# Performance work log

Measured on AMD Instinct MI355X. Metric: run time of the kernel, lower is better.

## Reference

```python
import jax, jax.numpy as jnp
import numpy as np

EMBED_DIM = 1024
NUM_HEADS = 16
HEAD_DIM = EMBED_DIM // NUM_HEADS


def setup_inputs() -> dict:
    key = jax.random.key(0)
    ks = jax.random.split(key, 8)
    B, S, D = 2, 2048, EMBED_DIM
    scale = 1.0 / np.sqrt(D)
    return {
        "query": jax.random.normal(ks[0], (B, S, D), dtype=jnp.float32),
        "key": jax.random.normal(ks[1], (B, S, D), dtype=jnp.float32),
        "value": jax.random.normal(ks[2], (B, S, D), dtype=jnp.float32),
        "Wq": jax.random.normal(ks[3], (D, D), dtype=jnp.float32) * scale,
        "Wk": jax.random.normal(ks[4], (D, D), dtype=jnp.float32) * scale,
        "Wv": jax.random.normal(ks[5], (D, D), dtype=jnp.float32) * scale,
        "Wo": jax.random.normal(ks[6], (D, D), dtype=jnp.float32) * scale,
        "attention_mask": jax.random.randint(ks[7], (B, S), 0, 2, dtype=jnp.int32),
    }


def reference(query, key, value, Wq, Wk, Wv, Wo, attention_mask):
    B, Sq, D = query.shape
    Sk = key.shape[1]
    H, hd = NUM_HEADS, HEAD_DIM
    # linear projections (no bias), split into heads: [B, H, S, hd]
    q = (query @ Wq).reshape(B, Sq, H, hd).transpose(0, 2, 1, 3)
    k = (key @ Wk).reshape(B, Sk, H, hd).transpose(0, 2, 1, 3)
    v = (value @ Wv).reshape(B, Sk, H, hd).transpose(0, 2, 1, 3)
    # scaled dot-product scores: [B, H, Sq, Sk]; scale uses head_dim (post-split key dim)
    scores = jnp.einsum("bhqd,bhkd->bhqk", q, k) / jnp.sqrt(jnp.float32(hd))
    # padding mask [B, Sk] broadcast to [B, 1, 1, Sk]; 0 -> -inf
    mask = attention_mask[:, None, None, :]
    scores = jnp.where(mask == 0, -jnp.inf, scores)
    weights = jax.nn.softmax(scores, axis=-1)
    out = jnp.einsum("bhqk,bhkd->bhqd", weights, v)  # [B, H, Sq, hd]
    out = out.transpose(0, 2, 1, 3).reshape(B, Sq, D)
    return out @ Wo
```

## Files before the change

### kernel.cpp

```cpp
#include <hip/hip_runtime.h>
#include <hip/hip_bf16.h>

typedef short bf16x8 __attribute__((ext_vector_type(8)));
typedef float f32x4 __attribute__((ext_vector_type(4)));

#define S_LEN 2048
#define NHEAD 16
#define DM 1024

#if __has_builtin(__builtin_amdgcn_exp2f)
#define EXP2(x) __builtin_amdgcn_exp2f(x)
#else
#define EXP2(x) exp2f(x)
#endif

__device__ __forceinline__ short f2bf(float f) {
  union { float f; unsigned u; } x; x.f = f;
  unsigned r = x.u + 0x7fffu + ((x.u >> 16) & 1u);
  return (short)(r >> 16);
}

__device__ __forceinline__ unsigned cvt_pk_bf16(float lo, float hi) {
  unsigned r;
  asm("v_cvt_pk_bf16_f32 %0, %1, %2" : "=v"(r) : "v"(lo), "v"(hi));
  return r;
}

__device__ __forceinline__ void pl32swap(unsigned& a, unsigned& b) {
#if __has_builtin(__builtin_amdgcn_permlane32_swap)
  auto r = __builtin_amdgcn_permlane32_swap(a, b, false, false);
  a = r[0]; b = r[1];
#else
  asm volatile("v_permlane32_swap_b32 %0, %1" : "+v"(a), "+v"(b));
#endif
}
__device__ __forceinline__ void pl16swap(unsigned& a, unsigned& b) {
#if __has_builtin(__builtin_amdgcn_permlane16_swap)
  auto r = __builtin_amdgcn_permlane16_swap(a, b, false, false);
  a = r[0]; b = r[1];
#else
  asm volatile("v_permlane16_swap_b32 %0, %1" : "+v"(a), "+v"(b));
#endif
}

__device__ __forceinline__ void gload16(const void* g, void* l) {
  __builtin_amdgcn_global_load_lds(
      (const __attribute__((address_space(1))) void*)g,
      (__attribute__((address_space(3))) void*)l, 16, 0, 0);
}

__global__ __launch_bounds__(256) void wtrans(const float* __restrict__ Wq, const float* __restrict__ Wk,
                                              const float* __restrict__ Wv, const float* __restrict__ Wo,
                                              short* Tq, short* Tk, short* Tv, short* To) {
  const int z = blockIdx.z;
  const float* W = (z == 0) ? Wq : (z == 1) ? Wk : (z == 2) ? Wv : Wo;
  short* T = (z == 0) ? Tq : (z == 1) ? Tk : (z == 2) ? Tv : To;
  __shared__ short Tl[64][72];
  const int tid = threadIdx.x;
  const int k0 = blockIdx.x * 64, n0 = blockIdx.y * 64;
  const int r = tid >> 2, c0 = (tid & 3) * 16;
#pragma unroll
  for (int j = 0; j < 4; j++) {
    float4 v = *(const float4*)&W[(size_t)(k0 + r) * DM + n0 + c0 + 4 * j];
    Tl[r][c0 + 4 * j + 0] = f2bf(v.x);
    Tl[r][c0 + 4 * j + 1] = f2bf(v.y);
    Tl[r][c0 + 4 * j + 2] = f2bf(v.z);
    Tl[r][c0 + 4 * j + 3] = f2bf(v.w);
  }
  __syncthreads();
  bf16x8 o0, o1;
#pragma unroll
  for (int j = 0; j < 8; j++) { o0[j] = Tl[c0 + j][r]; o1[j] = Tl[c0 + 8 + j][r]; }
  *(bf16x8*)&T[(size_t)(n0 + r) * DM + k0 + c0] = o0;
  *(bf16x8*)&T[(size_t)(n0 + r) * DM + k0 + c0 + 8] = o1;
}

__global__ __launch_bounds__(256) void xcvt(const float* __restrict__ q, const float* __restrict__ k,
                                            const float* __restrict__ v,
                                            short* xq, short* xk, short* xv) {
  const int z = blockIdx.y;
  const float* src = (z == 0) ? q : (z == 1) ? k : v;
  short* dst = (z == 0) ? xq : (z == 1) ? xk : xv;
  const size_t base = ((size_t)blockIdx.x * 256 + threadIdx.x) * 16;
  float4 a = *(const float4*)&src[base];
  float4 b = *(const float4*)&src[base + 4];
  float4 c = *(const float4*)&src[base + 8];
  float4 d = *(const float4*)&src[base + 12];
  bf16x8 o0, o1;
  o0[0] = f2bf(a.x); o0[1] = f2bf(a.y); o0[2] = f2bf(a.z); o0[3] = f2bf(a.w);
  o0[4] = f2bf(b.x); o0[5] = f2bf(b.y); o0[6] = f2bf(b.z); o0[7] = f2bf(b.w);
  o1[0] = f2bf(c.x); o1[1] = f2bf(c.y); o1[2] = f2bf(c.z); o1[3] = f2bf(c.w);
  o1[4] = f2bf(d.x); o1[5] = f2bf(d.y); o1[6] = f2bf(d.z); o1[7] = f2bf(d.w);
  *(bf16x8*)&dst[base] = o0;
  *(bf16x8*)&dst[base + 8] = o1;
}

template<int CM>
__global__ __launch_bounds__(256) void gemm3(const short* __restrict__ A, const short* __restrict__ Bt,
                                             void* __restrict__ Cp, int M, int N, int K) {
  __shared__ __align__(16) short Al[2][128 * 64];
  __shared__ __align__(16) short Bl[2][64 * 64];
  const int tid = threadIdx.x;
  const int lane = tid & 63, w = tid >> 6;
  const int wm = w >> 1, wn = w & 1;
  const int lr = lane & 15, g = lane >> 4;

  const int flat = blockIdx.y * gridDim.x + blockIdx.x;
  const int nwg = gridDim.x * gridDim.y;
  const int wid = (flat & 7) * (nwg >> 3) + (flat >> 3);
  const int bx = wid % gridDim.x, by = wid / gridDim.x;
  const int m0 = by * 128, n0 = bx * 64;

  f32x4 acc[4][2];
#pragma unroll
  for (int i = 0; i < 4; i++)
#pragma unroll
    for (int j = 0; j < 2; j++) acc[i][j] = (f32x4){0.f, 0.f, 0.f, 0.f};

  const int srow = lane >> 3;
  const int sch = (lane & 7) ^ (srow & 7);
  const short* gA = A + (size_t)(m0 + w * 32 + srow) * K + 8 * sch;
  const short* gB = Bt + (size_t)(n0 + w * 16 + srow) * K + 8 * sch;

#define STAGE(buf, kk)                                                              \
  do {                                                                              \
    _Pragma("unroll") for (int c = 0; c < 4; c++)                                   \
        gload16(gA + (size_t)c * 8 * K + (kk), &Al[buf][(w * 32 + c * 8) * 64]);    \
    _Pragma("unroll") for (int c = 0; c < 2; c++)                                   \
        gload16(gB + (size_t)c * 8 * K + (kk), &Bl[buf][(w * 16 + c * 8) * 64]);    \
  } while (0)

  const int nsteps = K >> 6;
  STAGE(0, 0);
  int buf = 0;
  for (int t = 0; t < nsteps; t++) {
    __syncthreads();
    if (t + 1 < nsteps) STAGE(buf ^ 1, (t + 1) << 6);
#pragma unroll
    for (int kc = 0; kc < 2; kc++) {
      bf16x8 af[4], bfr[2];
#pragma unroll
      for (int mt = 0; mt < 4; mt++) {
        int row = wm * 64 + mt * 16 + lr;
        af[mt] = *(const bf16x8*)&Al[buf][row * 64 + 8 * ((kc * 4 + g) ^ (lr & 7))];
      }
#pragma unroll
      for (int nt = 0; nt < 2; nt++) {
        int row = wn * 32 + nt * 16 + lr;
        bfr[nt] = *(const bf16x8*)&Bl[buf][row * 64 + 8 * ((kc * 4 + g) ^ (lr & 7))];
      }
      __builtin_amdgcn_s_setprio(1);
#pragma unroll
      for (int mt = 0; mt < 4; mt++)
#pragma unroll
        for (int nt = 0; nt < 2; nt++)
          acc[mt][nt] = __builtin_amdgcn_mfma_f32_16x16x32_bf16(af[mt], bfr[nt], acc[mt][nt], 0, 0, 0);
      __builtin_amdgcn_s_setprio(0);
    }
    buf ^= 1;
  }
#undef STAGE

#pragma unroll
  for (int mt = 0; mt < 4; mt++)
#pragma unroll
    for (int nt = 0; nt < 2; nt++)
#pragma unroll
      for (int r = 0; r < 4; r++) {
        int row = m0 + wm * 64 + mt * 16 + g * 4 + r;
        int col = n0 + wn * 32 + nt * 16 + lr;
        if (CM == 0) {
          ((float*)Cp)[(size_t)row * N + col] = acc[mt][nt][r];
        } else if (CM == 1 || CM == 3) {
          float v = (CM == 3) ? acc[mt][nt][r] * 0.18033688011f : acc[mt][nt][r];
          int b = row >> 11, s = row & (S_LEN - 1);
          int h = col >> 6, d = col & 63;
          ((short*)Cp)[(((size_t)(b * NHEAD + h)) * S_LEN + s) * 64 + d] = f2bf(v);
        } else {
          int h = row >> 6, d = row & 63;
          int b = col >> 11, s = col & (S_LEN - 1);
          ((short*)Cp)[(((size_t)(b * NHEAD + h)) * 64 + d) * S_LEN + s] = f2bf(acc[mt][nt][r]);
        }
      }
}

template<int AM, int BMODE, int CM>
__global__ __launch_bounds__(256) void gemm2(const void* __restrict__ Ap, const void* __restrict__ Bp,
                                             void* __restrict__ Cp, int M, int N, int K) {
  __shared__ __align__(16) short Al[128][72];
  __shared__ __align__(16) short Bl[64][72];
  const int tid = threadIdx.x;
  const int lane = tid & 63, w = tid >> 6;
  const int wm = w >> 1, wn = w & 1;
  const int lr = lane & 15, g = lane >> 4;
  const int m0 = blockIdx.y * 128, n0 = blockIdx.x * 64;

  f32x4 acc[4][2];
#pragma unroll
  for (int i = 0; i < 4; i++)
#pragma unroll
    for (int j = 0; j < 2; j++) acc[i][j] = (f32x4){0.f, 0.f, 0.f, 0.f};

  const int ar = tid >> 1, ac = (tid & 1) * 32;
  const int br = tid >> 2, bc = (tid & 3) * 16;

  float4 la[8]; bf16x8 la8[4];
  float4 lb[4]; bf16x8 lb8[2];

#define LOADA(kk)                                                                        \
  do {                                                                                   \
    if (AM == 0) {                                                                       \
      const float* A = (const float*)Ap;                                                 \
      _Pragma("unroll") for (int j = 0; j < 8; j++)                                      \
          la[j] = *(const float4*)&A[(size_t)(m0 + ar) * K + (kk) + ac + 4 * j];         \
    } else {                                                                             \
      const short* A = (const short*)Ap;                                                 \
      _Pragma("unroll") for (int j = 0; j < 4; j++)                                      \
          la8[j] = *(const bf16x8*)&A[(size_t)(m0 + ar) * K + (kk) + ac + 8 * j];        \
    }                                                                                    \
  } while (0)

#define LOADB(kk)                                                                        \
  do {                                                                                   \
    if (BMODE == 0) {                                                                    \
      const float* B = (const float*)Bp;                                                 \
      _Pragma("unroll") for (int j = 0; j < 4; j++)                                      \
          lb[j] = *(const float4*)&B[(size_t)(n0 + br) * K + (kk) + bc + 4 * j];         \
    } else if (BMODE == 1) {                                                             \
      const short* B = (const short*)Bp;                                                 \
      _Pragma("unroll") for (int j = 0; j < 2; j++)                                      \
          lb8[j] = *(const bf16x8*)&B[(size_t)(n0 + br) * K + (kk) + bc + 8 * j];        \
    } else {                                                                             \
      const float* B = (const float*)Bp;                                                 \
      _Pragma("unroll") for (int j = 0; j < 4; j++)                                      \
          lb[j] = *(const float4*)&B[(size_t)((kk) + br) * N + n0 + bc + 4 * j];         \
    }                                                                                    \
  } while (0)

  const int nsteps = K >> 6;
  LOADA(0); LOADB(0);

  for (int t = 0; t < nsteps; t++) {
    __syncthreads();
    if (AM == 0) {
#pragma unroll
      for (int j = 0; j < 4; j++) {
        float4 v0 = la[2 * j], v1 = la[2 * j + 1];
        bf16x8 tt;
        tt[0] = f2bf(v0.x); tt[1] = f2bf(v0.y); tt[2] = f2bf(v0.z); tt[3] = f2bf(v0.w);
        tt[4] = f2bf(v1.x); tt[5] = f2bf(v1.y); tt[6] = f2bf(v1.z); tt[7] = f2bf(v1.w);
        *(bf16x8*)&Al[ar][ac + 8 * j] = tt;
      }
    } else {
#pragma unroll
      for (int j = 0; j < 4; j++) *(bf16x8*)&Al[ar][ac + 8 * j] = la8[j];
    }
    if (BMODE == 0) {
#pragma unroll
      for (int j = 0; j < 2; j++) {
        float4 v0 = lb[2 * j], v1 = lb[2 * j + 1];
        bf16x8 tt;
        tt[0] = f2bf(v0.x); tt[1] = f2bf(v0.y); tt[2] = f2bf(v0.z); tt[3] = f2bf(v0.w);
        tt[4] = f2bf(v1.x); tt[5] = f2bf(v1.y); tt[6] = f2bf(v1.z); tt[7] = f2bf(v1.w);
        *(bf16x8*)&Bl[br][bc + 8 * j] = tt;
      }
    } else if (BMODE == 1) {
#pragma unroll
      for (int j = 0; j < 2; j++) *(bf16x8*)&Bl[br][bc + 8 * j] = lb8[j];
    } else {
#pragma unroll
      for (int j = 0; j < 4; j++) {
        float4 v = lb[j];
        Bl[bc + 4 * j + 0][br] = f2bf(v.x);
        Bl[bc + 4 * j + 1][br] = f2bf(v.y);
        Bl[bc + 4 * j + 2][br] = f2bf(v.z);
        Bl[bc + 4 * j + 3][br] = f2bf(v.w);
      }
    }
    __syncthreads();
    if (t + 1 < nsteps) { LOADA((t + 1) << 6); LOADB((t + 1) << 6); }
#pragma unroll
    for (int kc = 0; kc < 2; kc++) {
      bf16x8 af[4], bfr[2];
#pragma unroll
      for (int mt = 0; mt < 4; mt++) af[mt] = *(const bf16x8*)&Al[wm * 64 + mt * 16 + lr][kc * 32 + g * 8];
#pragma unroll
      for (int nt = 0; nt < 2; nt++) bfr[nt] = *(const bf16x8*)&Bl[wn * 32 + nt * 16 + lr][kc * 32 + g * 8];
#pragma unroll
      for (int mt = 0; mt < 4; mt++)
#pragma unroll
        for (int nt = 0; nt < 2; nt++)
          acc[mt][nt] = __builtin_amdgcn_mfma_f32_16x16x32_bf16(af[mt], bfr[nt], acc[mt][nt], 0, 0, 0);
    }
  }
#undef LOADA
#undef LOADB

#pragma unroll
  for (int mt = 0; mt < 4; mt++)
#pragma unroll
    for (int nt = 0; nt < 2; nt++)
#pragma unroll
      for (int r = 0; r < 4; r++) {
        int row = m0 + wm * 64 + mt * 16 + g * 4 + r;
        int col = n0 + wn * 32 + nt * 16 + lr;
        if (CM == 0) {
          ((float*)Cp)[(size_t)row * N + col] = acc[mt][nt][r];
        } else if (CM == 1 || CM == 3) {
          float v = (CM == 3) ? acc[mt][nt][r] * 0.18033688011f : acc[mt][nt][r];
          int b = row >> 11, s = row & (S_LEN - 1);
          int h = col >> 6, d = col & 63;
          ((short*)Cp)[(((size_t)(b * NHEAD + h)) * S_LEN + s) * 64 + d] = f2bf(v);
        } else {
          int h = row >> 6, d = row & 63;
          int b = col >> 11, s = col & (S_LEN - 1);
          ((short*)Cp)[(((size_t)(b * NHEAD + h)) * 64 + d) * S_LEN + s] = f2bf(acc[mt][nt][r]);
        }
      }
}

__global__ __launch_bounds__(256, 2) void attn6(const short* __restrict__ Qb,
                                                const short* __restrict__ Kb,
                                                const short* __restrict__ VbT,
                                                const int* __restrict__ mask,
                                                short* __restrict__ Ob) {
  __shared__ __align__(16) short Kl[2][64][64];
  __shared__ __align__(16) short Vl[2][64][64];

  const int tid = threadIdx.x;
  const int lane = tid & 63, w = tid >> 6;
  const int lr = lane & 15, g = lane >> 4;

  const int flat = blockIdx.y * gridDim.x + blockIdx.x;
  const int wid = (flat & 7) * 64 + (flat >> 3);
  const int qblk = wid & 15, bh = wid >> 4;
  const int b = bh >> 4, h = bh & 15;
  const int qbase = qblk * 128;
  const size_t hoff = (size_t)bh * S_LEN * 64;

  bf16x8 qf[2][2];
#pragma unroll
  for (int qfr = 0; qfr < 2; qfr++)
#pragma unroll
    for (int kh = 0; kh < 2; kh++)
      qf[qfr][kh] = *(const bf16x8*)&Qb[hoff + (size_t)(qbase + w * 32 + qfr * 16 + lr) * 64 + kh * 32 + g * 8];

  f32x4 o_acc[2][4];
  float lsum[2];
#pragma unroll
  for (int qfr = 0; qfr < 2; qfr++) {
    lsum[qfr] = 0.f;
#pragma unroll
    for (int dg = 0; dg < 4; dg++) o_acc[qfr][dg] = (f32x4){0.f, 0.f, 0.f, 0.f};
  }

  const int* maskb = mask + b * S_LEN;
  const int srow = lane >> 3;
  const int sch = (lane & 7) ^ (srow & 7);
  const short* gK = Kb + hoff + (size_t)(w * 16 + srow) * 64 + 8 * sch;
  const short* gV = VbT + hoff + (size_t)(w * 16 + srow) * S_LEN + 8 * sch;

#define STAGEKV(buf, kb)                                                         \
  do {                                                                           \
    _Pragma("unroll") for (int c = 0; c < 2; c++)                                \
        gload16(gK + (size_t)(kb + c * 8) * 64, &Kl[buf][w * 16 + c * 8][0]);    \
    _Pragma("unroll") for (int c = 0; c < 2; c++)                                \
        gload16(gV + (size_t)c * 8 * S_LEN + (kb), &Vl[buf][w * 16 + c * 8][0]); \
  } while (0)

  const int NT = S_LEN / 64;
  STAGEKV(0, 0);
  int buf = 0;

  for (int t = 0; t < NT; t++) {
    const int kb = t * 64;
    __syncthreads();
    if (t + 1 < NT) STAGEKV(buf ^ 1, kb + 64);

    float bias[4][4];
#pragma unroll
    for (int nt = 0; nt < 4; nt++) {
      int4 mv = *(const int4*)&maskb[kb + nt * 16 + 4 * g];
      bias[nt][0] = mv.x ? 0.f : -1e30f;
      bias[nt][1] = mv.y ? 0.f : -1e30f;
      bias[nt][2] = mv.z ? 0.f : -1e30f;
      bias[nt][3] = mv.w ? 0.f : -1e30f;
    }

    bf16x8 kfr[4][2];
#pragma unroll
    for (int nt = 0; nt < 4; nt++)
#pragma unroll
      for (int kh = 0; kh < 2; kh++)
        kfr[nt][kh] = *(const bf16x8*)&Kl[buf][nt * 16 + lr][8 * ((4 * kh + g) ^ (lr & 7))];

    bf16x8 vfr[4][2];
#pragma unroll
    for (int dg = 0; dg < 4; dg++)
#pragma unroll
      for (int kh = 0; kh < 2; kh++)
        vfr[dg][kh] = *(const bf16x8*)&Vl[buf][dg * 16 + lr][8 * ((4 * kh + g) ^ (lr & 7))];

#pragma unroll
    for (int qfr = 0; qfr < 2; qfr++) {
      f32x4 s[4];
#pragma unroll
      for (int nt = 0; nt < 4; nt++) s[nt] = (f32x4){0.f, 0.f, 0.f, 0.f};
      __builtin_amdgcn_s_setprio(1);
#pragma unroll
      for (int nt = 0; nt < 4; nt++) {
        s[nt] = __builtin_amdgcn_mfma_f32_16x16x32_bf16(kfr[nt][0], qf[qfr][0], s[nt], 0, 0, 0);
        s[nt] = __builtin_amdgcn_mfma_f32_16x16x32_bf16(kfr[nt][1], qf[qfr][1], s[nt], 0, 0, 0);
      }
      __builtin_amdgcn_s_setprio(0);

      unsigned W0[4], W1[4];
#pragma unroll
      for (int nt = 0; nt < 4; nt++) {
        float p0 = EXP2(s[nt][0] + bias[nt][0]);
        float p1 = EXP2(s[nt][1] + bias[nt][1]);
        float p2 = EXP2(s[nt][2] + bias[nt][2]);
        float p3 = EXP2(s[nt][3] + bias[nt][3]);
        lsum[qfr] += (p0 + p1) + (p2 + p3);
        W0[nt] = cvt_pk_bf16(p0, p1);
        W1[nt] = cvt_pk_bf16(p2, p3);
      }

      bf16x8 pf[2];
#pragma unroll
      for (int kh = 0; kh < 2; kh++) {
        unsigned a0 = W0[2 * kh], b0 = W0[2 * kh + 1];
        unsigned a1 = W1[2 * kh], b1 = W1[2 * kh + 1];
        pl32swap(a0, b0); pl16swap(a0, b0);
        pl32swap(a1, b1); pl16swap(a1, b1);
        union { unsigned u[4]; bf16x8 v; } pk;
        pk.u[0] = a0; pk.u[1] = a1; pk.u[2] = b0; pk.u[3] = b1;
        pf[kh] = pk.v;
      }

      __builtin_amdgcn_s_setprio(1);
#pragma unroll
      for (int dg = 0; dg < 4; dg++) {
        o_acc[qfr][dg] = __builtin_amdgcn_mfma_f32_16x16x32_bf16(pf[0], vfr[dg][0], o_acc[qfr][dg], 0, 0, 0);
        o_acc[qfr][dg] = __builtin_amdgcn_mfma_f32_16x16x32_bf16(pf[1], vfr[dg][1], o_acc[qfr][dg], 0, 0, 0);
      }
      __builtin_amdgcn_s_setprio(0);
    }
    buf ^= 1;
  }
#undef STAGEKV

#pragma unroll
  for (int qfr = 0; qfr < 2; qfr++) {
    float l = lsum[qfr];
    l += __shfl_xor(l, 16);
    l += __shfl_xor(l, 32);
    float inv = 1.f / l;
    float invq[4];
#pragma unroll
    for (int r = 0; r < 4; r++) invq[r] = __shfl(inv, 4 * g + r);
#pragma unroll
    for (int dg = 0; dg < 4; dg++)
#pragma unroll
      for (int r = 0; r < 4; r++) {
        int qr = qbase + w * 32 + qfr * 16 + 4 * g + r;
        int col = h * 64 + dg * 16 + lr;
        Ob[((size_t)b * S_LEN + qr) * DM + col] = f2bf(o_acc[qfr][dg][r] * invq[r]);
      }
  }
}

extern "C" void kernel_launch(void* const* d_in, const int* in_sizes, int n_in,
                              void* d_out, int out_size, void* d_ws, size_t ws_size,
                              hipStream_t stream) {
  const float* query = (const float*)d_in[0];
  const float* key   = (const float*)d_in[1];
  const float* value = (const float*)d_in[2];
  const float* Wq = (const float*)d_in[3];
  const float* Wk = (const float*)d_in[4];
  const float* Wv = (const float*)d_in[5];
  const float* Wo = (const float*)d_in[6];
  const int* mask = (const int*)d_in[7];

  char* ws = (char*)d_ws;
  const size_t MB = 1 << 20;
  const bool big = ws_size >= 41 * MB;

  dim3 ag(S_LEN / 128, 2 * NHEAD);

  if (big) {
    short* xq  = (short*)(ws);
    short* xk  = (short*)(ws + 8 * MB);
    short* xv  = (short*)(ws + 16 * MB);
    short* WqT = (short*)(ws + 24 * MB);
    short* WkT = (short*)(ws + 26 * MB);
    short* WvT = (short*)(ws + 28 * MB);
    short* WoT = (short*)(ws + 30 * MB);
    short* Qb  = (short*)(ws + 32 * MB);
    short* Kb  = xq;
    short* VbT = xk;
    short* Ob  = xv;

    dim3 tgrid(16, 16, 4);
    wtrans<<<tgrid, 256, 0, stream>>>(Wq, Wk, Wv, Wo, WqT, WkT, WvT, WoT);
    dim3 cg(1024, 3);
    xcvt<<<cg, 256, 0, stream>>>(query, key, value, xq, xk, xv);

    dim3 gqk(DM / 64, (2 * S_LEN) / 128);
    gemm3<3><<<gqk, 256, 0, stream>>>(xq, WqT, Qb, 2 * S_LEN, DM, DM);
    gemm3<1><<<gqk, 256, 0, stream>>>(xk, WkT, Kb, 2 * S_LEN, DM, DM);
    dim3 gv((2 * S_LEN) / 64, DM / 128);
    gemm3<2><<<gv, 256, 0, stream>>>(WvT, xv, VbT, DM, 2 * S_LEN, DM);

    attn6<<<ag, 256, 0, stream>>>(Qb, Kb, VbT, mask, Ob);

    gemm3<0><<<gqk, 256, 0, stream>>>(Ob, WoT, (float*)d_out, 2 * S_LEN, DM, DM);
  } else {
    short* Qb  = (short*)(ws);
    short* Kb  = (short*)(ws + 8 * MB);
    short* VbT = (short*)(ws + 16 * MB);
    short* WqT = (short*)(ws + 24 * MB);
    short* WkT = (short*)(ws + 26 * MB);
    short* WvT = (short*)(ws + 28 * MB);
    short* Ob  = (short*)(ws + 24 * MB);

    dim3 tgrid(16, 16, 3);
    wtrans<<<tgrid, 256, 0, stream>>>(Wq, Wk, Wv, Wo, WqT, WkT, WvT, WqT);

    dim3 gq(DM / 64, (2 * S_LEN) / 128);
    gemm2<0, 1, 3><<<gq, 256, 0, stream>>>(query, WqT, Qb, 2 * S_LEN, DM, DM);
    gemm2<0, 1, 1><<<gq, 256, 0, stream>>>(key,   WkT, Kb, 2 * S_LEN, DM, DM);
    dim3 gv((2 * S_LEN) / 64, DM / 128);
    gemm2<1, 0, 2><<<gv, 256, 0, stream>>>(WvT, value, VbT, DM, 2 * S_LEN, DM);

    attn6<<<ag, 256, 0, stream>>>(Qb, Kb, VbT, mask, Ob);

    gemm2<1, 2, 0><<<gq, 256, 0, stream>>>(Ob, Wo, (float*)d_out, 2 * S_LEN, DM, DM);
  }
}
```

Before: 137.4 us.

## Fuse fp32 conversion into a single QKV projection GEMM and retile attention

Replaces the separate fp32-to-bf16 conversion kernel and three projection GEMMs with one kernel, gemm4. It reads fp32 activations directly, converts them into LDS, and uses the concatenated transposed Wq/Wk/Wv weights to write Q (pre-scaled), K and transposed V. This removes the intermediate bf16 activation round trip through memory and several kernel launches. Attention is retiled from 128 to 64 queries per block, with one query fragment per wave and higher declared occupancy. That gives the grid more blocks to spread across CUs, at the cost of less reuse of each staged K/V tile.

```diff
diff --git a/kernel.cpp b/kernel.cpp
--- a/kernel.cpp
+++ b/kernel.cpp
@@ -75,24 +75,113 @@
   *(bf16x8*)&T[(size_t)(n0 + r) * DM + k0 + c0 + 8] = o1;
 }
 
-__global__ __launch_bounds__(256) void xcvt(const float* __restrict__ q, const float* __restrict__ k,
-                                            const float* __restrict__ v,
-                                            short* xq, short* xk, short* xv) {
-  const int z = blockIdx.y;
-  const float* src = (z == 0) ? q : (z == 1) ? k : v;
-  short* dst = (z == 0) ? xq : (z == 1) ? xk : xv;
-  const size_t base = ((size_t)blockIdx.x * 256 + threadIdx.x) * 16;
-  float4 a = *(const float4*)&src[base];
-  float4 b = *(const float4*)&src[base + 4];
-  float4 c = *(const float4*)&src[base + 8];
-  float4 d = *(const float4*)&src[base + 12];
-  bf16x8 o0, o1;
-  o0[0] = f2bf(a.x); o0[1] = f2bf(a.y); o0[2] = f2bf(a.z); o0[3] = f2bf(a.w);
-  o0[4] = f2bf(b.x); o0[5] = f2bf(b.y); o0[6] = f2bf(b.z); o0[7] = f2bf(b.w);
-  o1[0] = f2bf(c.x); o1[1] = f2bf(c.y); o1[2] = f2bf(c.z); o1[3] = f2bf(c.w);
-  o1[4] = f2bf(d.x); o1[5] = f2bf(d.y); o1[6] = f2bf(d.z); o1[7] = f2bf(d.w);
-  *(bf16x8*)&dst[base] = o0;
-  *(bf16x8*)&dst[base + 8] = o1;
+__global__ __launch_bounds__(256) void gemm4(const float* __restrict__ xq, const float* __restrict__ xk,
+                                             const float* __restrict__ xv, const short* __restrict__ Wt,
+                                             short* __restrict__ Qb, short* __restrict__ Kb,
+                                             short* __restrict__ VbT) {
+  __shared__ __align__(16) short Al[128 * 64];
+  __shared__ __align__(16) short Bl[2][64 * 64];
+  const int tid = threadIdx.x;
+  const int lane = tid & 63, w = tid >> 6;
+  const int wm = w >> 1, wn = w & 1;
+  const int lr = lane & 15, g = lane >> 4;
+
+  const int flat = blockIdx.y * gridDim.x + blockIdx.x;
+  const int wid = (flat & 7) * 192 + (flat >> 3);
+  const int bx = wid % 48, by = wid / 48;
+  const int n0 = bx * 64, m0 = by * 128;
+  const int which = n0 >> 10;
+  const float* A = (which == 0) ? xq : (which == 1) ? xk : xv;
+
+  f32x4 acc[4][2];
+#pragma unroll
+  for (int i = 0; i < 4; i++)
+#pragma unroll
+    for (int j = 0; j < 2; j++) acc[i][j] = (f32x4){0.f, 0.f, 0.f, 0.f};
+
+  const int ar = tid >> 1, ac = (tid & 1) * 32;
+  float4 la[8];
+  const int srow = lane >> 3;
+  const int sch = (lane & 7) ^ (srow & 7);
+  const short* gB = Wt + (size_t)(n0 + w * 16 + srow) * 1024 + 8 * sch;
+
+#define LOADA4(kk)                                                                  \
+  do {                                                                              \
+    _Pragma("unroll") for (int j = 0; j < 8; j++)                                   \
+        la[j] = *(const float4*)&A[(size_t)(m0 + ar) * 1024 + (kk) + ac + 4 * j];   \
+  } while (0)
+#define STAGEB(buf, kk)                                                             \
+  do {                                                                              \
+    _Pragma("unroll") for (int c = 0; c < 2; c++)                                   \
+        gload16(gB + (size_t)c * 8 * 1024 + (kk), &Bl[buf][(w * 16 + c * 8) * 64]); \
+  } while (0)
+
+  const int nsteps = 16;
+  LOADA4(0);
+  STAGEB(0, 0);
+  int buf = 0;
+  for (int t = 0; t < nsteps; t++) {
+    __syncthreads();
+#pragma unroll
+    for (int j = 0; j < 4; j++) {
+      float4 v0 = la[2 * j], v1 = la[2 * j + 1];
+      bf16x8 tt;
+      tt[0] = f2bf(v0.x); tt[1] = f2bf(v0.y); tt[2] = f2bf(v0.z); tt[3] = f2bf(v0.w);
+      tt[4] = f2bf(v1.x); tt[5] = f2bf(v1.y); tt[6] = f2bf(v1.z); tt[7] = f2bf(v1.w);
+      *(bf16x8*)&Al[ar * 64 + 8 * (((ac >> 3) + j) ^ (ar & 7))] = tt;
+    }
+    __syncthreads();
+    if (t + 1 < nsteps) { STAGEB(buf ^ 1, (t + 1) << 6); LOADA4((t + 1) << 6); }
+#pragma unroll
+    for (int kc = 0; kc < 2; kc++) {
+      bf16x8 af[4], bfr[2];
+#pragma unroll
+      for (int mt = 0; mt < 4; mt++) {
+        int row = wm * 64 + mt * 16 + lr;
+        af[mt] = *(const bf16x8*)&Al[row * 64 + 8 * ((kc * 4 + g) ^ (lr & 7))];
+      }
+#pragma unroll
+      for (int nt = 0; nt < 2; nt++) {
+        int row = wn * 32 + nt * 16 + lr;
+        bfr[nt] = *(const bf16x8*)&Bl[buf][row * 64 + 8 * ((kc * 4 + g) ^ (lr & 7))];
+      }
+      __builtin_amdgcn_s_setprio(1);
+#pragma unroll
+      for (int mt = 0; mt < 4; mt++)
+#pragma unroll
+        for (int nt = 0; nt < 2; nt++)
+          acc[mt][nt] = __builtin_amdgcn_mfma_f32_16x16x32_bf16(af[mt], bfr[nt], acc[mt][nt], 0, 0, 0);
+      __builtin_amdgcn_s_setprio(0);
+    }
+    buf ^= 1;
+  }
+#undef LOADA4
+#undef STAGEB
+
+  const int hcol = (n0 >> 6) & 15;
+#pragma unroll
+  for (int mt = 0; mt < 4; mt++)
+#pragma unroll
+    for (int nt = 0; nt < 2; nt++) {
+      const int d = wn * 32 + nt * 16 + lr;
+      if (which == 2) {
+        const int sb = m0 + wm * 64 + mt * 16 + g * 4;
+        const int bb = sb >> 11, s = sb & (S_LEN - 1);
+        union { short s4[4]; uint2 u; } pk;
+#pragma unroll
+        for (int r = 0; r < 4; r++) pk.s4[r] = f2bf(acc[mt][nt][r]);
+        *(uint2*)&VbT[(((size_t)(bb * NHEAD + hcol)) * 64 + d) * S_LEN + s] = pk.u;
+      } else {
+        short* dst = (which == 0) ? Qb : Kb;
+        const float scale = (which == 0) ? 0.18033688011f : 1.f;
+#pragma unroll
+        for (int r = 0; r < 4; r++) {
+          int row = m0 + wm * 64 + mt * 16 + g * 4 + r;
+          int bb = row >> 11, s = row & (S_LEN - 1);
+          dst[(((size_t)(bb * NHEAD + hcol)) * S_LEN + s) * 64 + d] = f2bf(acc[mt][nt][r] * scale);
+        }
+      }
+    }
 }
 
 template<int CM>
@@ -319,7 +408,7 @@
       }
 }
 
-__global__ __launch_bounds__(256, 2) void attn6(const short* __restrict__ Qb,
+__global__ __launch_bounds__(256, 4) void attn7(const short* __restrict__ Qb,
                                                 const short* __restrict__ Kb,
                                                 const short* __restrict__ VbT,
                                                 const int* __restrict__ mask,
@@ -332,27 +421,21 @@
   const int lr = lane & 15, g = lane >> 4;
 
   const int flat = blockIdx.y * gridDim.x + blockIdx.x;
-  const int wid = (flat & 7) * 64 + (flat >> 3);
-  const int qblk = wid & 15, bh = wid >> 4;
+  const int wid = (flat & 7) * 128 + (flat >> 3);
+  const int qblk = wid & 31, bh = wid >> 5;
   const int b = bh >> 4, h = bh & 15;
-  const int qbase = qblk * 128;
+  const int qbase = qblk * 64;
   const size_t hoff = (size_t)bh * S_LEN * 64;
 
-  bf16x8 qf[2][2];
-#pragma unroll
-  for (int qfr = 0; qfr < 2; qfr++)
-#pragma unroll
-    for (int kh = 0; kh < 2; kh++)
-      qf[qfr][kh] = *(const bf16x8*)&Qb[hoff + (size_t)(qbase + w * 32 + qfr * 16 + lr) * 64 + kh * 32 + g * 8];
-
-  f32x4 o_acc[2][4];
-  float lsum[2];
-#pragma unroll
-  for (int qfr = 0; qfr < 2; qfr++) {
-    lsum[qfr] = 0.f;
-#pragma unroll
-    for (int dg = 0; dg < 4; dg++) o_acc[qfr][dg] = (f32x4){0.f, 0.f, 0.f, 0.f};
-  }
+  bf16x8 qf[2];
+#pragma unroll
+  for (int kh = 0; kh < 2; kh++)
+    qf[kh] = *(const bf16x8*)&Qb[hoff + (size_t)(qbase + w * 16 + lr) * 64 + kh * 32 + g * 8];
+
+  f32x4 o_acc[4];
+  float lsum = 0.f;
+#pragma unroll
+  for (int dg = 0; dg < 4; dg++) o_acc[dg] = (f32x4){0.f, 0.f, 0.f, 0.f};
 
   const int* maskb = mask + b * S_LEN;
   const int srow = lane >> 3;
@@ -387,72 +470,58 @@
       bias[nt][3] = mv.w ? 0.f : -1e30f;
     }
 
-    bf16x8 kfr[4][2];
-#pragma unroll
-    for (int nt = 0; nt < 4; nt++)
-#pragma unroll
-      for (int kh = 0; kh < 2; kh++)
-        kfr[nt][kh] = *(const bf16x8*)&Kl[buf][nt * 16 + lr][8 * ((4 * kh + g) ^ (lr & 7))];
-
-    bf16x8 vfr[4][2];
-#pragma unroll
-    for (int dg = 0; dg < 4; dg++)
-#pragma unroll
-      for (int kh = 0; kh < 2; kh++)
-        vfr[dg][kh] = *(const bf16x8*)&Vl[buf][dg * 16 + lr][8 * ((4 * kh + g) ^ (lr & 7))];
-
-#pragma unroll
-    for (int qfr = 0; qfr < 2; qfr++) {
-      f32x4 s[4];
-#pragma unroll
-      for (int nt = 0; nt < 4; nt++) s[nt] = (f32x4){0.f, 0.f, 0.f, 0.f};
-      __builtin_amdgcn_s_setprio(1);
-#pragma unroll
-      for (int nt = 0; nt < 4; nt++) {
-        s[nt] = __builtin_amdgcn_mfma_f32_16x16x32_bf16(kfr[nt][0], qf[qfr][0], s[nt], 0, 0, 0);
-        s[nt] = __builtin_amdgcn_mfma_f32_16x16x32_bf16(kfr[nt][1], qf[qfr][1], s[nt], 0, 0, 0);
-      }
-      __builtin_amdgcn_s_setprio(0);
-
-      unsigned W0[4], W1[4];
-#pragma unroll
-      for (int nt = 0; nt < 4; nt++) {
-        float p0 = EXP2(s[nt][0] + bias[nt][0]);
-        float p1 = EXP2(s[nt][1] + bias[nt][1]);
-        float p2 = EXP2(s[nt][2] + bias[nt][2]);
-        float p3 = EXP2(s[nt][3] + bias[nt][3]);
-        lsum[qfr] += (p0 + p1) + (p2 + p3);
-        W0[nt] = cvt_pk_bf16(p0, p1);
-        W1[nt] = cvt_pk_bf16(p2, p3);
-      }
-
-      bf16x8 pf[2];
-#pragma unroll
-      for (int kh = 0; kh < 2; kh++) {
-        unsigned a0 = W0[2 * kh], b0 = W0[2 * kh + 1];
-        unsigned a1 = W1[2 * kh], b1 = W1[2 * kh + 1];
-        pl32swap(a0, b0); pl16swap(a0, b0);
-        pl32swap(a1, b1); pl16swap(a1, b1);
-        union { unsigned u[4]; bf16x8 v; } pk;
-        pk.u[0] = a0; pk.u[1] = a1; pk.u[2] = b0; pk.u[3] = b1;
-        pf[kh] = pk.v;
-      }
-
-      __builtin_amdgcn_s_setprio(1);
-#pragma unroll
-      for (int dg = 0; dg < 4; dg++) {
-        o_acc[qfr][dg] = __builtin_amdgcn_mfma_f32_16x16x32_bf16(pf[0], vfr[dg][0], o_acc[qfr][dg], 0, 0, 0);
-        o_acc[qfr][dg] = __builtin_amdgcn_mfma_f32_16x16x32_bf16(pf[1], vfr[dg][1], o_acc[qfr][dg], 0, 0, 0);
-      }
-      __builtin_amdgcn_s_setprio(0);
-    }
+    f32x4 s[4];
+#pragma unroll
+    for (int nt = 0; nt < 4; nt++) s[nt] = (f32x4){0.f, 0.f, 0.f, 0.f};
+    __builtin_amdgcn_s_setprio(1);
+#pragma unroll
+    for (int nt = 0; nt < 4; nt++) {
+      bf16x8 k0 = *(const bf16x8*)&Kl[buf][nt * 16 + lr][8 * (g ^ (lr & 7))];
+      bf16x8 k1 = *(const bf16x8*)&Kl[buf][nt * 16 + lr][8 * ((4 + g) ^ (lr & 7))];
+      s[nt] = __builtin_amdgcn_mfma_f32_16x16x32_bf16(k0, qf[0], s[nt], 0, 0, 0);
+      s[nt] = __builtin_amdgcn_mfma_f32_16x16x32_bf16(k1, qf[1], s[nt], 0, 0, 0);
+    }
+    __builtin_amdgcn_s_setprio(0);
+
+    unsigned W0[4], W1[4];
+#pragma unroll
+    for (int nt = 0; nt < 4; nt++) {
+      float p0 = EXP2(s[nt][0] + bias[nt][0]);
+      float p1 = EXP2(s[nt][1] + bias[nt][1]);
+      float p2 = EXP2(s[nt][2] + bias[nt][2]);
+      float p3 = EXP2(s[nt][3] + bias[nt][3]);
+      lsum += (p0 + p1) + (p2 + p3);
+      W0[nt] = cvt_pk_bf16(p0, p1);
+      W1[nt] = cvt_pk_bf16(p2, p3);
+    }
+
+    bf16x8 pf[2];
+#pragma unroll
+    for (int kh = 0; kh < 2; kh++) {
+      unsigned a0 = W0[2 * kh], b0 = W0[2 * kh + 1];
+      unsigned a1 = W1[2 * kh], b1 = W1[2 * kh + 1];
+      pl32swap(a0, b0); pl16swap(a0, b0);
+      pl32swap(a1, b1); pl16swap(a1, b1);
+      union { unsigned u[4]; bf16x8 v; } pk;
+      pk.u[0] = a0; pk.u[1] = a1; pk.u[2] = b0; pk.u[3] = b1;
+      pf[kh] = pk.v;
+    }
+
+    __builtin_amdgcn_s_setprio(1);
+#pragma unroll
+    for (int dg = 0; dg < 4; dg++) {
+      bf16x8 v0 = *(const bf16x8*)&Vl[buf][dg * 16 + lr][8 * (g ^ (lr & 7))];
+      bf16x8 v1 = *(const bf16x8*)&Vl[buf][dg * 16 + lr][8 * ((4 + g) ^ (lr & 7))];
+      o_acc[dg] = __builtin_amdgcn_mfma_f32_16x16x32_bf16(pf[0], v0, o_acc[dg], 0, 0, 0);
+      o_acc[dg] = __builtin_amdgcn_mfma_f32_16x16x32_bf16(pf[1], v1, o_acc[dg], 0, 0, 0);
+    }
+    __builtin_amdgcn_s_setprio(0);
     buf ^= 1;
   }
 #undef STAGEKV
 
-#pragma unroll
-  for (int qfr = 0; qfr < 2; qfr++) {
-    float l = lsum[qfr];
+  {
+    float l = lsum;
     l += __shfl_xor(l, 16);
     l += __shfl_xor(l, 32);
     float inv = 1.f / l;
@@ -463,9 +532,9 @@
     for (int dg = 0; dg < 4; dg++)
 #pragma unroll
       for (int r = 0; r < 4; r++) {
-        int qr = qbase + w * 32 + qfr * 16 + 4 * g + r;
+        int qr = qbase + w * 16 + 4 * g + r;
         int col = h * 64 + dg * 16 + lr;
-        Ob[((size_t)b * S_LEN + qr) * DM + col] = f2bf(o_acc[qfr][dg][r] * invq[r]);
+        Ob[((size_t)b * S_LEN + qr) * DM + col] = f2bf(o_acc[dg][r] * invq[r]);
       }
   }
 }
@@ -486,34 +555,27 @@
   const size_t MB = 1 << 20;
   const bool big = ws_size >= 41 * MB;
 
-  dim3 ag(S_LEN / 128, 2 * NHEAD);
+  dim3 ag(S_LEN / 64, 2 * NHEAD);
 
   if (big) {
-    short* xq  = (short*)(ws);
-    short* xk  = (short*)(ws + 8 * MB);
-    short* xv  = (short*)(ws + 16 * MB);
+    short* Qb  = (short*)(ws);
+    short* Kb  = (short*)(ws + 8 * MB);
+    short* VbT = (short*)(ws + 16 * MB);
     short* WqT = (short*)(ws + 24 * MB);
     short* WkT = (short*)(ws + 26 * MB);
     short* WvT = (short*)(ws + 28 * MB);
     short* WoT = (short*)(ws + 30 * MB);
-    short* Qb  = (short*)(ws + 32 * MB);
-    short* Kb  = xq;
-    short* VbT = xk;
-    short* Ob  = xv;
+    short* Ob  = (short*)(ws + 32 * MB);
 
     dim3 tgrid(16, 16, 4);
     wtrans<<<tgrid, 256, 0, stream>>>(Wq, Wk, Wv, Wo, WqT, WkT, WvT, WoT);
-    dim3 cg(1024, 3);
-    xcvt<<<cg, 256, 0, stream>>>(query, key, value, xq, xk, xv);
+
+    dim3 gqkv(48, 32);
+    gemm4<<<gqkv, 256, 0, stream>>>(query, key, value, WqT, Qb, Kb, VbT);
+
+    attn7<<<ag, 256, 0, stream>>>(Qb, Kb, VbT, mask, Ob);
 
     dim3 gqk(DM / 64, (2 * S_LEN) / 128);
-    gemm3<3><<<gqk, 256, 0, stream>>>(xq, WqT, Qb, 2 * S_LEN, DM, DM);
-    gemm3<1><<<gqk, 256, 0, stream>>>(xk, WkT, Kb, 2 * S_LEN, DM, DM);
-    dim3 gv((2 * S_LEN) / 64, DM / 128);
-    gemm3<2><<<gv, 256, 0, stream>>>(WvT, xv, VbT, DM, 2 * S_LEN, DM);
-
-    attn6<<<ag, 256, 0, stream>>>(Qb, Kb, VbT, mask, Ob);
-
     gemm3<0><<<gqk, 256, 0, stream>>>(Ob, WoT, (float*)d_out, 2 * S_LEN, DM, DM);
   } else {
     short* Qb  = (short*)(ws);
@@ -533,7 +595,7 @@
     dim3 gv((2 * S_LEN) / 64, DM / 128);
     gemm2<1, 0, 2><<<gv, 256, 0, stream>>>(WvT, value, VbT, DM, 2 * S_LEN, DM);
 
-    attn6<<<ag, 256, 0, stream>>>(Qb, Kb, VbT, mask, Ob);
+    attn7<<<ag, 256, 0, stream>>>(Qb, Kb, VbT, mask, Ob);
 
     gemm2<1, 2, 0><<<gq, 256, 0, stream>>>(Ob, Wo, (float*)d_out, 2 * S_LEN, DM, DM);
   }
```

Measured after the change: 188.1 us. +36.9%, slower.

## Shrink attention query tile and fold padding mask into V and MFMA denominator

Applied to the files above, without the earlier changes.

The attention kernel now handles 64 query rows per block, one 16-row fragment per wave, and allows 4 blocks per CU, so the grid doubles and per-thread register use drops. The padding mask is applied once in the V projection epilogue by zeroing masked value columns. It is also precomputed as a bf16 0/1 vector, and the softmax denominator comes from an extra MFMA against that vector instead of per-element bias adds and scalar row sums. This removes mask loads and adds from the inner loop, but each block now reuses each K/V tile for half as many query rows, which raises total K/V staging traffic. The small-workspace path gets a matching single-fragment kernel that keeps the bias-based masking.

```diff
diff --git a/kernel.cpp b/kernel.cpp
--- a/kernel.cpp
+++ b/kernel.cpp
@@ -51,12 +51,20 @@
 
 __global__ __launch_bounds__(256) void wtrans(const float* __restrict__ Wq, const float* __restrict__ Wk,
                                               const float* __restrict__ Wv, const float* __restrict__ Wo,
-                                              short* Tq, short* Tk, short* Tv, short* To) {
+                                              const int* __restrict__ mask,
+                                              short* Tq, short* Tk, short* Tv, short* To, short* Mb) {
   const int z = blockIdx.z;
+  const int tid = threadIdx.x;
+  if (z == 4) {
+    if (blockIdx.y == 0 && blockIdx.x < 16) {
+      int i = blockIdx.x * 256 + tid;
+      Mb[i] = mask[i] ? (short)0x3F80 : (short)0;
+    }
+    return;
+  }
   const float* W = (z == 0) ? Wq : (z == 1) ? Wk : (z == 2) ? Wv : Wo;
   short* T = (z == 0) ? Tq : (z == 1) ? Tk : (z == 2) ? Tv : To;
   __shared__ short Tl[64][72];
-  const int tid = threadIdx.x;
   const int k0 = blockIdx.x * 64, n0 = blockIdx.y * 64;
   const int r = tid >> 2, c0 = (tid & 3) * 16;
 #pragma unroll
@@ -97,7 +105,8 @@
 
 template<int CM>
 __global__ __launch_bounds__(256) void gemm3(const short* __restrict__ A, const short* __restrict__ Bt,
-                                             void* __restrict__ Cp, int M, int N, int K) {
+                                             void* __restrict__ Cp, int M, int N, int K,
+                                             const int* __restrict__ mask) {
   __shared__ __align__(16) short Al[2][128 * 64];
   __shared__ __align__(16) short Bl[2][64 * 64];
   const int tid = threadIdx.x;
@@ -164,24 +173,37 @@
 #pragma unroll
   for (int mt = 0; mt < 4; mt++)
 #pragma unroll
-    for (int nt = 0; nt < 2; nt++)
-#pragma unroll
-      for (int r = 0; r < 4; r++) {
-        int row = m0 + wm * 64 + mt * 16 + g * 4 + r;
-        int col = n0 + wn * 32 + nt * 16 + lr;
-        if (CM == 0) {
+    for (int nt = 0; nt < 2; nt++) {
+      if (CM == 0) {
+#pragma unroll
+        for (int r = 0; r < 4; r++) {
+          int row = m0 + wm * 64 + mt * 16 + g * 4 + r;
+          int col = n0 + wn * 32 + nt * 16 + lr;
           ((float*)Cp)[(size_t)row * N + col] = acc[mt][nt][r];
-        } else if (CM == 1 || CM == 3) {
-          float v = (CM == 3) ? acc[mt][nt][r] * 0.18033688011f : acc[mt][nt][r];
+        }
+      } else if (CM == 1 || CM == 3) {
+        const float scale = (CM == 3) ? 0.18033688011f : 1.f;
+#pragma unroll
+        for (int r = 0; r < 4; r++) {
+          int row = m0 + wm * 64 + mt * 16 + g * 4 + r;
+          int col = n0 + wn * 32 + nt * 16 + lr;
           int b = row >> 11, s = row & (S_LEN - 1);
           int h = col >> 6, d = col & 63;
-          ((short*)Cp)[(((size_t)(b * NHEAD + h)) * S_LEN + s) * 64 + d] = f2bf(v);
-        } else {
+          ((short*)Cp)[(((size_t)(b * NHEAD + h)) * S_LEN + s) * 64 + d] = f2bf(acc[mt][nt][r] * scale);
+        }
+      } else {
+#pragma unroll
+        for (int r = 0; r < 4; r++) {
+          int row = m0 + wm * 64 + mt * 16 + g * 4 + r;
+          int col = n0 + wn * 32 + nt * 16 + lr;
           int h = row >> 6, d = row & 63;
           int b = col >> 11, s = col & (S_LEN - 1);
-          ((short*)Cp)[(((size_t)(b * NHEAD + h)) * 64 + d) * S_LEN + s] = f2bf(acc[mt][nt][r]);
+          float v = acc[mt][nt][r];
+          if (CM == 4) v = mask[b * S_LEN + s] ? v : 0.f;
+          ((short*)Cp)[(((size_t)(b * NHEAD + h)) * 64 + d) * S_LEN + s] = f2bf(v);
         }
       }
+    }
 }
 
 template<int AM, int BMODE, int CM>
@@ -319,10 +341,10 @@
       }
 }
 
-__global__ __launch_bounds__(256, 2) void attn6(const short* __restrict__ Qb,
+__global__ __launch_bounds__(256, 4) void attn8(const short* __restrict__ Qb,
                                                 const short* __restrict__ Kb,
                                                 const short* __restrict__ VbT,
-                                                const int* __restrict__ mask,
+                                                const short* __restrict__ Mb,
                                                 short* __restrict__ Ob) {
   __shared__ __align__(16) short Kl[2][64][64];
   __shared__ __align__(16) short Vl[2][64][64];
@@ -332,29 +354,23 @@
   const int lr = lane & 15, g = lane >> 4;
 
   const int flat = blockIdx.y * gridDim.x + blockIdx.x;
-  const int wid = (flat & 7) * 64 + (flat >> 3);
-  const int qblk = wid & 15, bh = wid >> 4;
+  const int wid = (flat & 7) * 128 + (flat >> 3);
+  const int qblk = wid & 31, bh = wid >> 5;
   const int b = bh >> 4, h = bh & 15;
-  const int qbase = qblk * 128;
+  const int qbase = qblk * 64;
   const size_t hoff = (size_t)bh * S_LEN * 64;
 
-  bf16x8 qf[2][2];
-#pragma unroll
-  for (int qfr = 0; qfr < 2; qfr++)
-#pragma unroll
-    for (int kh = 0; kh < 2; kh++)
-      qf[qfr][kh] = *(const bf16x8*)&Qb[hoff + (size_t)(qbase + w * 32 + qfr * 16 + lr) * 64 + kh * 32 + g * 8];
-
-  f32x4 o_acc[2][4];
-  float lsum[2];
-#pragma unroll
-  for (int qfr = 0; qfr < 2; qfr++) {
-    lsum[qfr] = 0.f;
-#pragma unroll
-    for (int dg = 0; dg < 4; dg++) o_acc[qfr][dg] = (f32x4){0.f, 0.f, 0.f, 0.f};
-  }
-
-  const int* maskb = mask + b * S_LEN;
+  bf16x8 qf[2];
+#pragma unroll
+  for (int kh = 0; kh < 2; kh++)
+    qf[kh] = *(const bf16x8*)&Qb[hoff + (size_t)(qbase + w * 16 + lr) * 64 + kh * 32 + g * 8];
+
+  f32x4 o_acc[4];
+  f32x4 o_l = (f32x4){0.f, 0.f, 0.f, 0.f};
+#pragma unroll
+  for (int dg = 0; dg < 4; dg++) o_acc[dg] = (f32x4){0.f, 0.f, 0.f, 0.f};
+
+  const short* Mbb = Mb + b * S_LEN;
   const int srow = lane >> 3;
   const int sch = (lane & 7) ^ (srow & 7);
   const short* gK = Kb + hoff + (size_t)(w * 16 + srow) * 64 + 8 * sch;
@@ -374,6 +390,123 @@
 
   for (int t = 0; t < NT; t++) {
     const int kb = t * 64;
+    bf16x8 mf0 = *(const bf16x8*)&Mbb[kb + g * 8];
+    bf16x8 mf1 = *(const bf16x8*)&Mbb[kb + 32 + g * 8];
+    __syncthreads();
+    if (t + 1 < NT) STAGEKV(buf ^ 1, kb + 64);
+
+    f32x4 s[4];
+#pragma unroll
+    for (int nt = 0; nt < 4; nt++) s[nt] = (f32x4){0.f, 0.f, 0.f, 0.f};
+    __builtin_amdgcn_s_setprio(1);
+#pragma unroll
+    for (int nt = 0; nt < 4; nt++) {
+      bf16x8 k0 = *(const bf16x8*)&Kl[buf][nt * 16 + lr][8 * (g ^ (lr & 7))];
+      bf16x8 k1 = *(const bf16x8*)&Kl[buf][nt * 16 + lr][8 * ((4 + g) ^ (lr & 7))];
+      s[nt] = __builtin_amdgcn_mfma_f32_16x16x32_bf16(k0, qf[0], s[nt], 0, 0, 0);
+      s[nt] = __builtin_amdgcn_mfma_f32_16x16x32_bf16(k1, qf[1], s[nt], 0, 0, 0);
+    }
+    __builtin_amdgcn_s_setprio(0);
+
+    unsigned W0[4], W1[4];
+#pragma unroll
+    for (int nt = 0; nt < 4; nt++) {
+      float p0 = EXP2(s[nt][0]);
+      float p1 = EXP2(s[nt][1]);
+      float p2 = EXP2(s[nt][2]);
+      float p3 = EXP2(s[nt][3]);
+      W0[nt] = cvt_pk_bf16(p0, p1);
+      W1[nt] = cvt_pk_bf16(p2, p3);
+    }
+
+    bf16x8 pf[2];
+#pragma unroll
+    for (int kh = 0; kh < 2; kh++) {
+      unsigned a0 = W0[2 * kh], b0 = W0[2 * kh + 1];
+      unsigned a1 = W1[2 * kh], b1 = W1[2 * kh + 1];
+      pl32swap(a0, b0); pl16swap(a0, b0);
+      pl32swap(a1, b1); pl16swap(a1, b1);
+      union { unsigned u[4]; bf16x8 v; } pk;
+      pk.u[0] = a0; pk.u[1] = a1; pk.u[2] = b0; pk.u[3] = b1;
+      pf[kh] = pk.v;
+    }
+
+    __builtin_amdgcn_s_setprio(1);
+#pragma unroll
+    for (int dg = 0; dg < 4; dg++) {
+      bf16x8 v0 = *(const bf16x8*)&Vl[buf][dg * 16 + lr][8 * (g ^ (lr & 7))];
+      bf16x8 v1 = *(const bf16x8*)&Vl[buf][dg * 16 + lr][8 * ((4 + g) ^ (lr & 7))];
+      o_acc[dg] = __builtin_amdgcn_mfma_f32_16x16x32_bf16(pf[0], v0, o_acc[dg], 0, 0, 0);
+      o_acc[dg] = __builtin_amdgcn_mfma_f32_16x16x32_bf16(pf[1], v1, o_acc[dg], 0, 0, 0);
+    }
+    o_l = __builtin_amdgcn_mfma_f32_16x16x32_bf16(pf[0], mf0, o_l, 0, 0, 0);
+    o_l = __builtin_amdgcn_mfma_f32_16x16x32_bf16(pf[1], mf1, o_l, 0, 0, 0);
+    __builtin_amdgcn_s_setprio(0);
+    buf ^= 1;
+  }
+#undef STAGEKV
+
+#pragma unroll
+  for (int r = 0; r < 4; r++) {
+    float inv = 1.f / o_l[r];
+    int qr = qbase + w * 16 + 4 * g + r;
+#pragma unroll
+    for (int dg = 0; dg < 4; dg++) {
+      int col = h * 64 + dg * 16 + lr;
+      Ob[((size_t)b * S_LEN + qr) * DM + col] = f2bf(o_acc[dg][r] * inv);
+    }
+  }
+}
+
+__global__ __launch_bounds__(256, 4) void attn7(const short* __restrict__ Qb,
+                                                const short* __restrict__ Kb,
+                                                const short* __restrict__ VbT,
+                                                const int* __restrict__ mask,
+                                                short* __restrict__ Ob) {
+  __shared__ __align__(16) short Kl[2][64][64];
+  __shared__ __align__(16) short Vl[2][64][64];
+
+  const int tid = threadIdx.x;
+  const int lane = tid & 63, w = tid >> 6;
+  const int lr = lane & 15, g = lane >> 4;
+
+  const int flat = blockIdx.y * gridDim.x + blockIdx.x;
+  const int wid = (flat & 7) * 128 + (flat >> 3);
+  const int qblk = wid & 31, bh = wid >> 5;
+  const int b = bh >> 4, h = bh & 15;
+  const int qbase = qblk * 64;
+  const size_t hoff = (size_t)bh * S_LEN * 64;
+
+  bf16x8 qf[2];
+#pragma unroll
+  for (int kh = 0; kh < 2; kh++)
+    qf[kh] = *(const bf16x8*)&Qb[hoff + (size_t)(qbase + w * 16 + lr) * 64 + kh * 32 + g * 8];
+
+  f32x4 o_acc[4];
+  float lsum = 0.f;
+#pragma unroll
+  for (int dg = 0; dg < 4; dg++) o_acc[dg] = (f32x4){0.f, 0.f, 0.f, 0.f};
+
+  const int* maskb = mask + b * S_LEN;
+  const int srow = lane >> 3;
+  const int sch = (lane & 7) ^ (srow & 7);
+  const short* gK = Kb + hoff + (size_t)(w * 16 + srow) * 64 + 8 * sch;
+  const short* gV = VbT + hoff + (size_t)(w * 16 + srow) * S_LEN + 8 * sch;
+
+#define STAGEKV(buf, kb)                                                         \
+  do {                                                                           \
+    _Pragma("unroll") for (int c = 0; c < 2; c++)                                \
+        gload16(gK + (size_t)(kb + c * 8) * 64, &Kl[buf][w * 16 + c * 8][0]);    \
+    _Pragma("unroll") for (int c = 0; c < 2; c++)                                \
+        gload16(gV + (size_t)c * 8 * S_LEN + (kb), &Vl[buf][w * 16 + c * 8][0]); \
+  } while (0)
+
+  const int NT = S_LEN / 64;
+  STAGEKV(0, 0);
+  int buf = 0;
+
+  for (int t = 0; t < NT; t++) {
+    const int kb = t * 64;
     __syncthreads();
     if (t + 1 < NT) STAGEKV(buf ^ 1, kb + 64);
 
@@ -387,72 +520,58 @@
       bias[nt][3] = mv.w ? 0.f : -1e30f;
     }
 
-    bf16x8 kfr[4][2];
-#pragma unroll
-    for (int nt = 0; nt < 4; nt++)
-#pragma unroll
-      for (int kh = 0; kh < 2; kh++)
-        kfr[nt][kh] = *(const bf16x8*)&Kl[buf][nt * 16 + lr][8 * ((4 * kh + g) ^ (lr & 7))];
-
-    bf16x8 vfr[4][2];
-#pragma unroll
-    for (int dg = 0; dg < 4; dg++)
-#pragma unroll
-      for (int kh = 0; kh < 2; kh++)
-        vfr[dg][kh] = *(const bf16x8*)&Vl[buf][dg * 16 + lr][8 * ((4 * kh + g) ^ (lr & 7))];
-
-#pragma unroll
-    for (int qfr = 0; qfr < 2; qfr++) {
-      f32x4 s[4];
-#pragma unroll
-      for (int nt = 0; nt < 4; nt++) s[nt] = (f32x4){0.f, 0.f, 0.f, 0.f};
-      __builtin_amdgcn_s_setprio(1);
-#pragma unroll
-      for (int nt = 0; nt < 4; nt++) {
-        s[nt] = __builtin_amdgcn_mfma_f32_16x16x32_bf16(kfr[nt][0], qf[qfr][0], s[nt], 0, 0, 0);
-        s[nt] = __builtin_amdgcn_mfma_f32_16x16x32_bf16(kfr[nt][1], qf[qfr][1], s[nt], 0, 0, 0);
-      }
-      __builtin_amdgcn_s_setprio(0);
-
-      unsigned W0[4], W1[4];
-#pragma unroll
-      for (int nt = 0; nt < 4; nt++) {
-        float p0 = EXP2(s[nt][0] + bias[nt][0]);
-        float p1 = EXP2(s[nt][1] + bias[nt][1]);
-        float p2 = EXP2(s[nt][2] + bias[nt][2]);
-        float p3 = EXP2(s[nt][3] + bias[nt][3]);
-        lsum[qfr] += (p0 + p1) + (p2 + p3);
-        W0[nt] = cvt_pk_bf16(p0, p1);
-        W1[nt] = cvt_pk_bf16(p2, p3);
-      }
-
-      bf16x8 pf[2];
-#pragma unroll
-      for (int kh = 0; kh < 2; kh++) {
-        unsigned a0 = W0[2 * kh], b0 = W0[2 * kh + 1];
-        unsigned a1 = W1[2 * kh], b1 = W1[2 * kh + 1];
-        pl32swap(a0, b0); pl16swap(a0, b0);
-        pl32swap(a1, b1); pl16swap(a1, b1);
-        union { unsigned u[4]; bf16x8 v; } pk;
-        pk.u[0] = a0; pk.u[1] = a1; pk.u[2] = b0; pk.u[3] = b1;
-        pf[kh] = pk.v;
-      }
-
-      __builtin_amdgcn_s_setprio(1);
-#pragma unroll
-      for (int dg = 0; dg < 4; dg++) {
-        o_acc[qfr][dg] = __builtin_amdgcn_mfma_f32_16x16x32_bf16(pf[0], vfr[dg][0], o_acc[qfr][dg], 0, 0, 0);
-        o_acc[qfr][dg] = __builtin_amdgcn_mfma_f32_16x16x32_bf16(pf[1], vfr[dg][1], o_acc[qfr][dg], 0, 0, 0);
-      }
-      __builtin_amdgcn_s_setprio(0);
-    }
+    f32x4 s[4];
+#pragma unroll
+    for (int nt = 0; nt < 4; nt++) s[nt] = (f32x4){0.f, 0.f, 0.f, 0.f};
+    __builtin_amdgcn_s_setprio(1);
+#pragma unroll
+    for (int nt = 0; nt < 4; nt++) {
+      bf16x8 k0 = *(const bf16x8*)&Kl[buf][nt * 16 + lr][8 * (g ^ (lr & 7))];
+      bf16x8 k1 = *(const bf16x8*)&Kl[buf][nt * 16 + lr][8 * ((4 + g) ^ (lr & 7))];
+      s[nt] = __builtin_amdgcn_mfma_f32_16x16x32_bf16(k0, qf[0], s[nt], 0, 0, 0);
+      s[nt] = __builtin_amdgcn_mfma_f32_16x16x32_bf16(k1, qf[1], s[nt], 0, 0, 0);
+    }
+    __builtin_amdgcn_s_setprio(0);
+
+    unsigned W0[4], W1[4];
+#pragma unroll
+    for (int nt = 0; nt < 4; nt++) {
+      float p0 = EXP2(s[nt][0] + bias[nt][0]);
+      float p1 = EXP2(s[nt][1] + bias[nt][1]);
+      float p2 = EXP2(s[nt][2] + bias[nt][2]);
+      float p3 = EXP2(s[nt][3] + bias[nt][3]);
+      lsum += (p0 + p1) + (p2 + p3);
+      W0[nt] = cvt_pk_bf16(p0, p1);
+      W1[nt] = cvt_pk_bf16(p2, p3);
+    }
+
+    bf16x8 pf[2];
+#pragma unroll
+    for (int kh = 0; kh < 2; kh++) {
+      unsigned a0 = W0[2 * kh], b0 = W0[2 * kh + 1];
+      unsigned a1 = W1[2 * kh], b1 = W1[2 * kh + 1];
+      pl32swap(a0, b0); pl16swap(a0, b0);
+      pl32swap(a1, b1); pl16swap(a1, b1);
+      union { unsigned u[4]; bf16x8 v; } pk;
+      pk.u[0] = a0; pk.u[1] = a1; pk.u[2] = b0; pk.u[3] = b1;
+      pf[kh] = pk.v;
+    }
+
+    __builtin_amdgcn_s_setprio(1);
+#pragma unroll
+    for (int dg = 0; dg < 4; dg++) {
+      bf16x8 v0 = *(const bf16x8*)&Vl[buf][dg * 16 + lr][8 * (g ^ (lr & 7))];
+      bf16x8 v1 = *(const bf16x8*)&Vl[buf][dg * 16 + lr][8 * ((4 + g) ^ (lr & 7))];
+      o_acc[dg] = __builtin_amdgcn_mfma_f32_16x16x32_bf16(pf[0], v0, o_acc[dg], 0, 0, 0);
+      o_acc[dg] = __builtin_amdgcn_mfma_f32_16x16x32_bf16(pf[1], v1, o_acc[dg], 0, 0, 0);
+    }
+    __builtin_amdgcn_s_setprio(0);
     buf ^= 1;
   }
 #undef STAGEKV
 
-#pragma unroll
-  for (int qfr = 0; qfr < 2; qfr++) {
-    float l = lsum[qfr];
+  {
+    float l = lsum;
     l += __shfl_xor(l, 16);
     l += __shfl_xor(l, 32);
     float inv = 1.f / l;
@@ -463,9 +582,9 @@
     for (int dg = 0; dg < 4; dg++)
 #pragma unroll
       for (int r = 0; r < 4; r++) {
-        int qr = qbase + w * 32 + qfr * 16 + 4 * g + r;
+        int qr = qbase + w * 16 + 4 * g + r;
         int col = h * 64 + dg * 16 + lr;
-        Ob[((size_t)b * S_LEN + qr) * DM + col] = f2bf(o_acc[qfr][dg][r] * invq[r]);
+        Ob[((size_t)b * S_LEN + qr) * DM + col] = f2bf(o_acc[dg][r] * invq[r]);
       }
   }
 }
@@ -486,7 +605,7 @@
   const size_t MB = 1 << 20;
   const bool big = ws_size >= 41 * MB;
 
-  dim3 ag(S_LEN / 128, 2 * NHEAD);
+  dim3 ag(S_LEN / 64, 2 * NHEAD);
 
   if (big) {
     short* xq  = (short*)(ws);
@@ -497,24 +616,25 @@
     short* WvT = (short*)(ws + 28 * MB);
     short* WoT = (short*)(ws + 30 * MB);
     short* Qb  = (short*)(ws + 32 * MB);
+    short* Mb  = (short*)(ws + 40 * MB);
     short* Kb  = xq;
     short* VbT = xk;
     short* Ob  = xv;
 
-    dim3 tgrid(16, 16, 4);
-    wtrans<<<tgrid, 256, 0, stream>>>(Wq, Wk, Wv, Wo, WqT, WkT, WvT, WoT);
+    dim3 tgrid(16, 16, 5);
+    wtrans<<<tgrid, 256, 0, stream>>>(Wq, Wk, Wv, Wo, mask, WqT, WkT, WvT, WoT, Mb);
     dim3 cg(1024, 3);
     xcvt<<<cg, 256, 0, stream>>>(query, key, value, xq, xk, xv);
 
     dim3 gqk(DM / 64, (2 * S_LEN) / 128);
-    gemm3<3><<<gqk, 256, 0, stream>>>(xq, WqT, Qb, 2 * S_LEN, DM, DM);
-    gemm3<1><<<gqk, 256, 0, stream>>>(xk, WkT, Kb, 2 * S_LEN, DM, DM);
+    gemm3<3><<<gqk, 256, 0, stream>>>(xq, WqT, Qb, 2 * S_LEN, DM, DM, mask);
+    gemm3<1><<<gqk, 256, 0, stream>>>(xk, WkT, Kb, 2 * S_LEN, DM, DM, mask);
     dim3 gv((2 * S_LEN) / 64, DM / 128);
-    gemm3<2><<<gv, 256, 0, stream>>>(WvT, xv, VbT, DM, 2 * S_LEN, DM);
-
-    attn6<<<ag, 256, 0, stream>>>(Qb, Kb, VbT, mask, Ob);
-
-    gemm3<0><<<gqk, 256, 0, stream>>>(Ob, WoT, (float*)d_out, 2 * S_LEN, DM, DM);
+    gemm3<4><<<gv, 256, 0, stream>>>(WvT, xv, VbT, DM, 2 * S_LEN, DM, mask);
+
+    attn8<<<ag, 256, 0, stream>>>(Qb, Kb, VbT, Mb, Ob);
+
+    gemm3<0><<<gqk, 256, 0, stream>>>(Ob, WoT, (float*)d_out, 2 * S_LEN, DM, DM, mask);
   } else {
     short* Qb  = (short*)(ws);
     short* Kb  = (short*)(ws + 8 * MB);
@@ -525,7 +645,7 @@
     short* Ob  = (short*)(ws + 24 * MB);
 
     dim3 tgrid(16, 16, 3);
-    wtrans<<<tgrid, 256, 0, stream>>>(Wq, Wk, Wv, Wo, WqT, WkT, WvT, WqT);
+    wtrans<<<tgrid, 256, 0, stream>>>(Wq, Wk, Wv, Wo, mask, WqT, WkT, WvT, WqT, WqT);
 
     dim3 gq(DM / 64, (2 * S_LEN) / 128);
     gemm2<0, 1, 3><<<gq, 256, 0, stream>>>(query, WqT, Qb, 2 * S_LEN, DM, DM);
@@ -533,7 +653,7 @@
     dim3 gv((2 * S_LEN) / 64, DM / 128);
     gemm2<1, 0, 2><<<gv, 256, 0, stream>>>(WvT, value, VbT, DM, 2 * S_LEN, DM);
 
-    attn6<<<ag, 256, 0, stream>>>(Qb, Kb, VbT, mask, Ob);
+    attn7<<<ag, 256, 0, stream>>>(Qb, Kb, VbT, mask, Ob);
 
     gemm2<1, 2, 0><<<gq, 256, 0, stream>>>(Ob, Wo, (float*)d_out, 2 * S_LEN, DM, DM);
   }
```

Result: no change. 138.5 us (median of 3 runs) (+0.8%).
